# Optimization experiments

Hardware: AMD Instinct MI355X
Metric: run time of the kernel (lower is better)

The kernel has to match this reference:

```python
import jax, jax.numpy as jnp
import numpy as np

BATCH_SIZE = 4096
N_VIEWS = 2
NUM_GPU = 1
TEMPERATURE = 0.07
FEAT_DIM = 128
N = (BATCH_SIZE // NUM_GPU) * N_VIEWS  # 8192


def setup_inputs() -> dict:
    key = jax.random.key(0)
    features = jax.random.normal(key, (N, FEAT_DIM), dtype=jnp.float32)
    return {"features": features}


def reference(features):
    n = features.shape[0]
    b = BATCH_SIZE // NUM_GPU
    # labels: [arange(b)] * n_views concatenated -> pairwise equality matrix
    lbl_vec = jnp.tile(jnp.arange(b), N_VIEWS)            # [N]
    lab = lbl_vec[None, :] == lbl_vec[:, None]            # [N, N] bool

    # F.normalize(dim=1): divide by L2 norm clamped at 1e-12
    norm = jnp.linalg.norm(features, axis=1, keepdims=True)
    f = features / jnp.maximum(norm, 1e-12)
    sim = f @ f.T                                          # [N, N]

    # Remove diagonal: row i keeps columns j != i in original order.
    cols = jnp.arange(n - 1)
    off_idx = cols[None, :] + (cols[None, :] >= jnp.arange(n)[:, None])  # [N, N-1]
    sim_od = jnp.take_along_axis(sim, off_idx, axis=1)     # [N, N-1]
    lab_od = jnp.take_along_axis(lab, off_idx, axis=1)     # [N, N-1] bool

    # Stable sort: positives (label True) first, preserving original column order,
    # matching torch's masked-select + concat([positives, negatives]).
    order = jnp.argsort(~lab_od, axis=1, stable=True)      # [N, N-1]
    logits = jnp.take_along_axis(sim_od, order, axis=1) / TEMPERATURE

    # CrossEntropyLoss with target class 0 (mean reduction)
    loss = -jax.nn.log_softmax(logits, axis=1)[:, 0]
    return loss.mean()
```

## Files before the change

kernel.cpp:

```cpp
#include <hip/hip_runtime.h>
#include <hip/hip_bf16.h>
#include <cstdint>

#define NROWS 8192
#define FDIM  128
#define HALF_N 4096

typedef short bf16x8 __attribute__((ext_vector_type(8)));
typedef float f32x4  __attribute__((ext_vector_type(4)));

#define K1 (1.4426950408889634f / 0.07f)

#if __has_builtin(__builtin_amdgcn_exp2f)
#define EXP2(x) __builtin_amdgcn_exp2f(x)
#else
#define EXP2(x) exp2f(x)
#endif

#define NBLK_TRI 1056


__global__ void __launch_bounds__(256) normalize_kernel(const float* __restrict__ f,
                                                        short* __restrict__ packed,
                                                        float* __restrict__ esum_g) {
    const int row  = blockIdx.x * 4 + (threadIdx.x >> 6);
    const int lane = threadIdx.x & 63;
    const float2 v = ((const float2*)(f + (size_t)row * FDIM))[lane];
    float ss = v.x * v.x + v.y * v.y;
    #pragma unroll
    for (int m = 1; m < 64; m <<= 1) ss += __shfl_xor(ss, m);
    const float scale = 1.0f / fmaxf(sqrtf(ss), 1e-12f);

    const int off = ((((row >> 4) * 4 + (lane >> 4)) * 64)
                     + ((lane >> 2) & 3) * 16 + (row & 15)) * 8 + 2 * (lane & 3);
    __hip_bfloat16 b0 = __float2bfloat16(v.x * scale);
    __hip_bfloat16 b1 = __float2bfloat16(v.y * scale);
    unsigned u = (unsigned)*(unsigned short*)&b0
               | ((unsigned)*(unsigned short*)&b1 << 16);
    *(unsigned*)(packed + off) = u;

    if (threadIdx.x < 4) esum_g[blockIdx.x * 4 + threadIdx.x] = 0.0f;
}

__device__ __forceinline__ float2 bf2_to_f2(unsigned u) {
    return make_float2(__uint_as_float(u << 16),
                       __uint_as_float(u & 0xffff0000u));
}

__global__ void __launch_bounds__(256, 4) sim_kernel(const short* __restrict__ pk,
                                                     float* __restrict__ esum_g,
                                                     float* __restrict__ pos_g,
                                                     float* __restrict__ diag_g) {
    if (blockIdx.x >= NBLK_TRI) {
        const int i  = (blockIdx.x - NBLK_TRI) * 256 + threadIdx.x;
        const int ip = i ^ HALF_N;
        const uint4* P = (const uint4*)pk;
        float dot = 0.f, self = 0.f;
        #pragma unroll
        for (int cc = 0; cc < 16; cc++) {
            const uint4 a = P[((i  >> 4) * 4 + (cc >> 2)) * 64 + (cc & 3) * 16 + (i  & 15)];
            const uint4 b = P[((ip >> 4) * 4 + (cc >> 2)) * 64 + (cc & 3) * 16 + (ip & 15)];
            const unsigned au[4] = {a.x, a.y, a.z, a.w};
            const unsigned bu[4] = {b.x, b.y, b.z, b.w};
            #pragma unroll
            for (int q = 0; q < 4; q++) {
                const float2 av = bf2_to_f2(au[q]);
                const float2 bv = bf2_to_f2(bu[q]);
                dot  = __builtin_fmaf(av.x, bv.x, __builtin_fmaf(av.y, bv.y, dot));
                self = __builtin_fmaf(av.x, av.x, __builtin_fmaf(av.y, av.y, self));
            }
        }
        pos_g[i]  = dot;
        diag_g[i] = EXP2(__builtin_fmaf(self, K1, -K1));
        return;
    }

    const int t = blockIdx.x;
    int J = (int)((sqrtf(4.0f * (float)t + 1.0f) - 1.0f) * 0.5f);
    while ((J + 1) * (J + 2) <= t) J++;
    while (J * (J + 1) > t) J--;
    const int rb = t - J * (J + 1);
    const bool upper = rb < 2 * J;

    const int tid   = threadIdx.x;
    const int w     = tid >> 6;
    const int lane  = tid & 63;
    const int quad  = lane >> 4;
    const int l16   = lane & 15;
    const int strip = rb * 4 + w;
    const bf16x8* P = (const bf16x8*)pk;

    __shared__ float colsum[256];
    colsum[tid] = 0.0f;

    bf16x8 a_reg[4][2];
    #pragma unroll
    for (int fr = 0; fr < 2; fr++)
        #pragma unroll
        for (int ks = 0; ks < 4; ks++)
            a_reg[ks][fr] = P[(((strip * 2 + fr) * 4) + ks) * 64 + lane];

    float ep[2][4];
    #pragma unroll
    for (int a = 0; a < 2; a++)
        #pragma unroll
        for (int b = 0; b < 4; b++) ep[a][b] = 0.0f;

    __syncthreads();

    const int cb0 = J * 16;

    #pragma unroll 8
    for (int cb = 0; cb < 16; cb++) {
        bf16x8 b[4];
        #pragma unroll
        for (int ks = 0; ks < 4; ks++)
            b[ks] = P[((cb0 + cb) * 4 + ks) * 64 + lane];

        f32x4 acc[2];
        #pragma unroll
        for (int fr = 0; fr < 2; fr++) acc[fr] = (f32x4){0.f, 0.f, 0.f, 0.f};
        #pragma unroll
        for (int ks = 0; ks < 4; ks++)
            #pragma unroll
            for (int fr = 0; fr < 2; fr++)
                acc[fr] = __builtin_amdgcn_mfma_f32_16x16x32_bf16(
                              a_reg[ks][fr], b[ks], acc[fr], 0, 0, 0);

        float cs = 0.0f;
        #pragma unroll
        for (int fr = 0; fr < 2; fr++)
            #pragma unroll
            for (int r = 0; r < 4; r++) {
                const float e = EXP2(__builtin_fmaf(acc[fr][r], K1, -K1));
                ep[fr][r] += e;
                cs += e;
            }

        if (upper) {
            cs += __shfl_xor(cs, 16);
            cs += __shfl_xor(cs, 32);
            if (quad == 0)
                atomicAdd(&colsum[cb * 16 + l16], cs);
        }
    }

    #pragma unroll
    for (int fr = 0; fr < 2; fr++)
        #pragma unroll
        for (int r = 0; r < 4; r++) {
            float v = ep[fr][r];
            #pragma unroll
            for (int m = 1; m < 16; m <<= 1) v += __shfl_xor(v, m);
            if (l16 == 0)
                atomicAdd(&esum_g[strip * 32 + fr * 16 + quad * 4 + r], v);
        }

    __syncthreads();
    if (upper) atomicAdd(&esum_g[J * 256 + tid], colsum[tid]);
}

__global__ void __launch_bounds__(256) final_kernel(const float* __restrict__ esum_g,
                                                    const float* __restrict__ pos_g,
                                                    const float* __restrict__ diag_g,
                                                    float* __restrict__ out) {
    const int tid = threadIdx.x;
    const float invT = 1.0f / 0.07f;
    float acc = 0.0f;
    for (int i = tid; i < NROWS; i += 256)
        acc += logf(esum_g[i] - diag_g[i]) + invT - pos_g[i] * invT;
    #pragma unroll
    for (int m = 1; m < 64; m <<= 1) acc += __shfl_xor(acc, m);
    __shared__ float ws[4];
    if ((tid & 63) == 0) ws[tid >> 6] = acc;
    __syncthreads();
    if (tid == 0) out[0] = (ws[0] + ws[1] + ws[2] + ws[3]) * (1.0f / (float)NROWS);
}

extern "C" void kernel_launch(void* const* d_in, const int* in_sizes, int n_in,
                              void* d_out, int out_size, void* d_ws, size_t ws_size,
                              hipStream_t stream) {
    const float* features = (const float*)d_in[0];
    float* out = (float*)d_out;

    char* ws = (char*)d_ws;
    short* packed = (short*)ws;
    float* esum_g = (float*)(ws + 2097152);
    float* pos_g  = (float*)(ws + 2097152 + 32768);
    float* diag_g = (float*)(ws + 2097152 + 65536);

    normalize_kernel<<<NROWS / 4, 256, 0, stream>>>(features, packed, esum_g);

    sim_kernel<<<NBLK_TRI + NROWS / 256, 256, 0, stream>>>(packed, esum_g, pos_g, diag_g);

    final_kernel<<<1, 256, 0, stream>>>(esum_g, pos_g, diag_g, out);
}
```

Baseline: 92.71 us.

## Fuse normalize, similarity and final reduction into one cooperative kernel

```diff
diff --git a/kernel.cpp b/kernel.cpp
--- a/kernel.cpp
+++ b/kernel.cpp
@@ -1,6 +1,9 @@
 #include <hip/hip_runtime.h>
+#include <hip/hip_cooperative_groups.h>
 #include <hip/hip_bf16.h>
 #include <cstdint>
+
+namespace cg = cooperative_groups;
 
 #define NROWS 8192
 #define FDIM  128
@@ -18,7 +21,170 @@
 #endif
 
 #define NBLK_TRI 1056
-
+#define NBLK_ALL (NBLK_TRI + 32)
+
+__device__ __forceinline__ float2 bf2_to_f2(unsigned u) {
+    return make_float2(__uint_as_float(u << 16),
+                       __uint_as_float(u & 0xffff0000u));
+}
+
+__global__ void __launch_bounds__(256, 4) fused_kernel(const float* __restrict__ f,
+                                                       short* __restrict__ packed,
+                                                       float* __restrict__ esum_g,
+                                                       float* __restrict__ pos_g,
+                                                       float* __restrict__ diag_g,
+                                                       float* __restrict__ out) {
+    const int tid  = threadIdx.x;
+    const int w    = tid >> 6;
+    const int lane = tid & 63;
+
+    {
+        const int gw = blockIdx.x * 4 + w;
+        #pragma unroll
+        for (int rep = 0; rep < 2; rep++) {
+            const int row = gw * 2 + rep;
+            const float2 v = ((const float2*)(f + (size_t)row * FDIM))[lane];
+            float ss = v.x * v.x + v.y * v.y;
+            #pragma unroll
+            for (int m = 1; m < 64; m <<= 1) ss += __shfl_xor(ss, m);
+            const float scale = 1.0f / fmaxf(sqrtf(ss), 1e-12f);
+
+            const int off = ((((row >> 4) * 4 + (lane >> 4)) * 64)
+                             + ((lane >> 2) & 3) * 16 + (row & 15)) * 8 + 2 * (lane & 3);
+            __hip_bfloat16 b0 = __float2bfloat16(v.x * scale);
+            __hip_bfloat16 b1 = __float2bfloat16(v.y * scale);
+            unsigned u = (unsigned)*(unsigned short*)&b0
+                       | ((unsigned)*(unsigned short*)&b1 << 16);
+            *(unsigned*)(packed + off) = u;
+        }
+        if (blockIdx.x < 32) esum_g[blockIdx.x * 256 + tid] = 0.0f;
+    }
+
+    cg::grid_group grid = cg::this_grid();
+    grid.sync();
+
+    const int quad = lane >> 4;
+    const int l16  = lane & 15;
+    const bf16x8* P = (const bf16x8*)packed;
+    __shared__ float colsum[256];
+
+    for (int vb = blockIdx.x; vb < NBLK_ALL; vb += 1024) {
+        if (vb >= NBLK_TRI) {
+            const int i  = (vb - NBLK_TRI) * 256 + tid;
+            const int ip = i ^ HALF_N;
+            const uint4* P4 = (const uint4*)packed;
+            float dot = 0.f, self = 0.f;
+            #pragma unroll
+            for (int cc = 0; cc < 16; cc++) {
+                const uint4 a = P4[((i  >> 4) * 4 + (cc >> 2)) * 64 + (cc & 3) * 16 + (i  & 15)];
+                const uint4 b = P4[((ip >> 4) * 4 + (cc >> 2)) * 64 + (cc & 3) * 16 + (ip & 15)];
+                const unsigned au[4] = {a.x, a.y, a.z, a.w};
+                const unsigned bu[4] = {b.x, b.y, b.z, b.w};
+                #pragma unroll
+                for (int q = 0; q < 4; q++) {
+                    const float2 av = bf2_to_f2(au[q]);
+                    const float2 bv = bf2_to_f2(bu[q]);
+                    dot  = __builtin_fmaf(av.x, bv.x, __builtin_fmaf(av.y, bv.y, dot));
+                    self = __builtin_fmaf(av.x, av.x, __builtin_fmaf(av.y, av.y, self));
+                }
+            }
+            pos_g[i]  = dot;
+            diag_g[i] = EXP2(__builtin_fmaf(self, K1, -K1));
+            continue;
+        }
+
+        const int t = vb;
+        int J = (int)((sqrtf(4.0f * (float)t + 1.0f) - 1.0f) * 0.5f);
+        while ((J + 1) * (J + 2) <= t) J++;
+        while (J * (J + 1) > t) J--;
+        const int rb = t - J * (J + 1);
+        const bool upper = rb < 2 * J;
+
+        const int strip = rb * 4 + w;
+        colsum[tid] = 0.0f;
+
+        bf16x8 a_reg[4][2];
+        #pragma unroll
+        for (int fr = 0; fr < 2; fr++)
+            #pragma unroll
+            for (int ks = 0; ks < 4; ks++)
+                a_reg[ks][fr] = P[(((strip * 2 + fr) * 4) + ks) * 64 + lane];
+
+        float ep[2][4];
+        #pragma unroll
+        for (int a = 0; a < 2; a++)
+            #pragma unroll
+            for (int b = 0; b < 4; b++) ep[a][b] = 0.0f;
+
+        __syncthreads();
+
+        const int cb0 = J * 16;
+
+        #pragma unroll 8
+        for (int cb = 0; cb < 16; cb++) {
+            bf16x8 b[4];
+            #pragma unroll
+            for (int ks = 0; ks < 4; ks++)
+                b[ks] = P[((cb0 + cb) * 4 + ks) * 64 + lane];
+
+            f32x4 acc[2];
+            #pragma unroll
+            for (int fr = 0; fr < 2; fr++) acc[fr] = (f32x4){0.f, 0.f, 0.f, 0.f};
+            #pragma unroll
+            for (int ks = 0; ks < 4; ks++)
+                #pragma unroll
+                for (int fr = 0; fr < 2; fr++)
+                    acc[fr] = __builtin_amdgcn_mfma_f32_16x16x32_bf16(
+                                  a_reg[ks][fr], b[ks], acc[fr], 0, 0, 0);
+
+            float cs = 0.0f;
+            #pragma unroll
+            for (int fr = 0; fr < 2; fr++)
+                #pragma unroll
+                for (int r = 0; r < 4; r++) {
+                    const float e = EXP2(__builtin_fmaf(acc[fr][r], K1, -K1));
+                    ep[fr][r] += e;
+                    cs += e;
+                }
+
+            if (upper) {
+                cs += __shfl_xor(cs, 16);
+                cs += __shfl_xor(cs, 32);
+                if (quad == 0)
+                    atomicAdd(&colsum[cb * 16 + l16], cs);
+            }
+        }
+
+        #pragma unroll
+        for (int fr = 0; fr < 2; fr++)
+            #pragma unroll
+            for (int r = 0; r < 4; r++) {
+                float v = ep[fr][r];
+                #pragma unroll
+                for (int m = 1; m < 16; m <<= 1) v += __shfl_xor(v, m);
+                if (l16 == 0)
+                    atomicAdd(&esum_g[strip * 32 + fr * 16 + quad * 4 + r], v);
+            }
+
+        __syncthreads();
+        if (upper) atomicAdd(&esum_g[J * 256 + tid], colsum[tid]);
+    }
+
+    grid.sync();
+
+    if (blockIdx.x == 0) {
+        const float invT = 1.0f / 0.07f;
+        float acc = 0.0f;
+        for (int i = tid; i < NROWS; i += 256)
+            acc += logf(esum_g[i] - diag_g[i]) + invT - pos_g[i] * invT;
+        #pragma unroll
+        for (int m = 1; m < 64; m <<= 1) acc += __shfl_xor(acc, m);
+        __shared__ float ws[4];
+        if ((tid & 63) == 0) ws[tid >> 6] = acc;
+        __syncthreads();
+        if (tid == 0) out[0] = (ws[0] + ws[1] + ws[2] + ws[3]) * (1.0f / (float)NROWS);
+    }
+}
 
 __global__ void __launch_bounds__(256) normalize_kernel(const float* __restrict__ f,
                                                         short* __restrict__ packed,
@@ -40,11 +206,6 @@
     *(unsigned*)(packed + off) = u;
 
     if (threadIdx.x < 4) esum_g[blockIdx.x * 4 + threadIdx.x] = 0.0f;
-}
-
-__device__ __forceinline__ float2 bf2_to_f2(unsigned u) {
-    return make_float2(__uint_as_float(u << 16),
-                       __uint_as_float(u & 0xffff0000u));
 }
 
 __global__ void __launch_bounds__(256, 4) sim_kernel(const short* __restrict__ pk,
@@ -189,9 +350,14 @@
     float* pos_g  = (float*)(ws + 2097152 + 32768);
     float* diag_g = (float*)(ws + 2097152 + 65536);
 
-    normalize_kernel<<<NROWS / 4, 256, 0, stream>>>(features, packed, esum_g);
-
-    sim_kernel<<<NBLK_TRI + NROWS / 256, 256, 0, stream>>>(packed, esum_g, pos_g, diag_g);
-
-    final_kernel<<<1, 256, 0, stream>>>(esum_g, pos_g, diag_g, out);
-}
+    void* kargs[] = {(void*)&features, (void*)&packed, (void*)&esum_g,
+                     (void*)&pos_g, (void*)&diag_g, (void*)&out};
+    hipError_t err = hipLaunchCooperativeKernel((void*)fused_kernel,
+                                                dim3(1024), dim3(256),
+                                                kargs, 0, stream);
+    if (err != hipSuccess) {
+        normalize_kernel<<<NROWS / 4, 256, 0, stream>>>(features, packed, esum_g);
+        sim_kernel<<<NBLK_ALL, 256, 0, stream>>>(packed, esum_g, pos_g, diag_g);
+        final_kernel<<<1, 256, 0, stream>>>(esum_g, pos_g, diag_g, out);
+    }
+}
```

Result: slower. 349.3 us (+276.8%).
